# Kernel optimization log

Hardware: AMD Instinct MI355X
Metric: run time of the kernel (lower is better)

The kernel has to match this reference:

```python
import jax, jax.numpy as jnp
import numpy as np

N_HEAD = 16
D_MODEL = 1024
D_HEAD = D_MODEL // N_HEAD
B, T = 2, 2048


def setup_inputs() -> dict:
    key = jax.random.key(0)
    k1, k2, k3 = jax.random.split(key, 3)
    x = jax.random.normal(k1, (B, T, D_MODEL), dtype=jnp.float32)
    w_attn = jax.random.normal(k2, (3 * D_MODEL, D_MODEL), dtype=jnp.float32) * (D_MODEL ** -0.5)
    w_proj = jax.random.normal(k3, (D_MODEL, D_MODEL), dtype=jnp.float32) * (D_MODEL ** -0.5)
    return {"x": x, "w_attn": w_attn, "w_proj": w_proj}


def _rms_norm(x):
    eps = jnp.asarray(jnp.finfo(x.dtype).eps, x.dtype)
    var = jnp.mean(jnp.square(x), axis=-1, keepdims=True)
    return x * jax.lax.rsqrt(var + eps)


def _rotate_half(x):
    x1, x2 = jnp.split(x, 2, axis=-1)
    return jnp.concatenate((-x2, x1), axis=-1)


def reference(x, w_attn, w_proj):
    Bx, Tx, C = x.shape
    qkv = jnp.einsum('btc,fc->btf', x, w_attn)  # [B,T,3C]
    q, k, v = jnp.split(qkv, 3, axis=-1)
    # [B, H, T, Dh]
    q = q.reshape(Bx, Tx, N_HEAD, D_HEAD).transpose(0, 2, 1, 3)
    k = k.reshape(Bx, Tx, N_HEAD, D_HEAD).transpose(0, 2, 1, 3)
    v = v.reshape(Bx, Tx, N_HEAD, D_HEAD).transpose(0, 2, 1, 3)
    # QK RMSNorm (no learned weight)
    q = _rms_norm(q)
    k = _rms_norm(k)
    # Rotary embedding over full d_head: freqs tiled twice
    inv_freq = 1.0 / (10000.0 ** (jnp.arange(0, D_HEAD, 2, dtype=jnp.float32) / D_HEAD))
    t = jnp.arange(Tx, dtype=jnp.float32)
    freqs = jnp.einsum('i,j->ij', t, inv_freq)  # [T, Dh/2]
    emb = jnp.concatenate((freqs, freqs), axis=-1)  # [T, Dh]
    cos = jnp.cos(emb)[None, None, :, :]
    sin = jnp.sin(emb)[None, None, :, :]
    q = q * cos + _rotate_half(q) * sin
    k = k * cos + _rotate_half(k) * sin
    # Causal SDPA
    scale = D_HEAD ** -0.5
    scores = jnp.einsum('bhqd,bhkd->bhqk', q, k) * scale
    causal = jnp.tril(jnp.ones((Tx, Tx), dtype=bool))
    scores = jnp.where(causal[None, None], scores, jnp.asarray(-jnp.inf, scores.dtype))
    attn = jax.nn.softmax(scores, axis=-1)
    y = jnp.einsum('bhqk,bhkd->bhqd', attn, v)
    y = y.transpose(0, 2, 1, 3).reshape(Bx, Tx, C)
    return jnp.einsum('btc,oc->bto', y, w_proj)
```

## Files before the change

kernel.cpp:

```cpp
#include <hip/hip_runtime.h>
#include <cstdint>
#include <cstddef>


typedef short bf16x8 __attribute__((ext_vector_type(8)));
typedef float floatx4 __attribute__((ext_vector_type(4)));
typedef unsigned short ushortx8 __attribute__((ext_vector_type(8)));
typedef unsigned short ushortx4 __attribute__((ext_vector_type(4)));

#define DEVI __device__ __forceinline__

DEVI float bf2f(unsigned short u) {
    unsigned int x = ((unsigned int)u) << 16;
    return __builtin_bit_cast(float, x);
}
DEVI unsigned short f2bf(float f) {
    unsigned int u = __builtin_bit_cast(unsigned int, f);
    u += 0x7fffu + ((u >> 16) & 1u);
    return (unsigned short)(u >> 16);
}

DEVI void glds16(const unsigned short* g, unsigned short* l) {
    __builtin_amdgcn_global_load_lds(
        (const __attribute__((address_space(1))) unsigned int*)g,
        (__attribute__((address_space(3))) unsigned int*)l, 16, 0, 0);
}

DEVI void cast8(unsigned short* dst, const float* src) {
    floatx4 a = *(const floatx4*)src;
    floatx4 b = *(const floatx4*)(src + 4);
    ushortx8 o;
    o[0] = f2bf(a[0]); o[1] = f2bf(a[1]); o[2] = f2bf(a[2]); o[3] = f2bf(a[3]);
    o[4] = f2bf(b[0]); o[5] = f2bf(b[1]); o[6] = f2bf(b[2]); o[7] = f2bf(b[3]);
    *(ushortx8*)dst = o;
}

__global__ __launch_bounds__(256)
void cast_inputs(const float* __restrict__ x, const float* __restrict__ wa,
                 const float* __restrict__ wp,
                 unsigned short* __restrict__ xb, unsigned short* __restrict__ wab,
                 unsigned short* __restrict__ wpb)
{
    size_t g = (size_t)blockIdx.x * 256 + threadIdx.x;
    size_t stride = (size_t)gridDim.x * 256;
    for (size_t i = g; i < (4194304 / 8); i += stride) cast8(xb  + i * 8, x  + i * 8);
    for (size_t i = g; i < (3145728 / 8); i += stride) cast8(wab + i * 8, wa + i * 8);
    for (size_t i = g; i < (1048576 / 8); i += stride) cast8(wpb + i * 8, wp + i * 8);
}

template <bool QKV_SPLIT, int BN>
__global__ __launch_bounds__(256)
void gemm_bt(const unsigned short* __restrict__ A, const unsigned short* __restrict__ B,
             unsigned short* __restrict__ Cqk, float* __restrict__ Cf,
             unsigned short* __restrict__ Vt, int M, int N, int K)
{
    constexpr int WCOLS = (BN == 128) ? 2 : 1;
    constexpr int WROWS = 4 / WCOLS;
    constexpr int MI    = 128 / (16 * WROWS);

    __shared__ __align__(16) unsigned short As[128 * 32];
    __shared__ __align__(16) unsigned short Bs[BN * 32];

    const int tid  = threadIdx.x;
    const int lane = tid & 63;
    const int w    = tid >> 6;
    const int wm   = w / WCOLS, wn = w % WCOLS;
    const int quad = lane >> 4;
    const int lm   = lane & 15;
    const int m0 = blockIdx.y * 128;
    const int n0 = blockIdx.x * BN;
    const int sr = lane >> 2;
    const int sc = (lane & 3) * 8;

    floatx4 acc[MI][4] = {};

    for (int k0 = 0; k0 < K; k0 += 32) {
        __syncthreads();
        #pragma unroll
        for (int i = 0; i < 2; ++i) {
            int r = w * 32 + i * 16;
            glds16(&A[(size_t)(m0 + r + sr) * K + k0 + sc], &As[r * 32]);
        }
        #pragma unroll
        for (int i = 0; i < BN / 64; ++i) {
            int r = w * (BN / 4) + i * 16;
            glds16(&B[(size_t)(n0 + r + sr) * K + k0 + sc], &Bs[r * 32]);
        }
        __syncthreads();

        bf16x8 a[MI];
        #pragma unroll
        for (int i = 0; i < MI; ++i)
            a[i] = *(const bf16x8*)&As[(wm * (16 * MI) + i * 16 + lm) * 32 + quad * 8];
        #pragma unroll
        for (int j = 0; j < 4; ++j) {
            bf16x8 b = *(const bf16x8*)&Bs[(wn * 64 + j * 16 + lm) * 32 + quad * 8];
            #pragma unroll
            for (int i = 0; i < MI; ++i)
                acc[i][j] = __builtin_amdgcn_mfma_f32_16x16x32_bf16(a[i], b, acc[i][j], 0, 0, 0);
        }
    }

    #pragma unroll
    for (int i = 0; i < MI; ++i) {
        #pragma unroll
        for (int j = 0; j < 4; ++j) {
            int col = n0 + wn * 64 + j * 16 + lm;
            #pragma unroll
            for (int r = 0; r < 4; ++r) {
                int row = m0 + wm * (16 * MI) + i * 16 + quad * 4 + r;
                if constexpr (QKV_SPLIT) {
                    unsigned short v = f2bf(acc[i][j][r]);
                    if (col < 2048) {
                        Cqk[(size_t)row * 2048 + col] = v;
                    } else {
                        int bq = row >> 11, t = row & 2047;
                        Vt[((size_t)(bq * 1024 + (col - 2048))) * 2048 + t] = v;
                    }
                } else {
                    Cf[(size_t)row * N + col] = acc[i][j][r];
                }
            }
        }
    }
}

__global__ __launch_bounds__(256)
void rmsnorm_rope(unsigned short* __restrict__ qk)
{
    int gw   = (blockIdx.x * 256 + threadIdx.x) >> 6;
    int lane = threadIdx.x & 63;
    int h = gw & 15;
    int t = (gw >> 4) & 2047;
    int b = gw >> 15;

    size_t base = ((size_t)(b * 2048 + t)) * 2048 + h * 64 + lane;
    float q = bf2f(qk[base]);
    float k = bf2f(qk[base + 1024]);

    float sq = q * q, sk = k * k;
    #pragma unroll
    for (int off = 32; off >= 1; off >>= 1) {
        sq += __shfl_xor(sq, off, 64);
        sk += __shfl_xor(sk, off, 64);
    }
    const float eps = 1.1920929e-07f;
    q *= rsqrtf(sq * (1.0f / 64.0f) + eps);
    k *= rsqrtf(sk * (1.0f / 64.0f) + eps);

    int i = lane & 31;
    float ang = (float)t * expf(-(float)i * 0.28782313662425572f);
    float c = cosf(ang), s = sinf(ang);
    float qp = __shfl_xor(q, 32, 64);
    float kp = __shfl_xor(k, 32, 64);
    float sgn = (lane < 32) ? -1.0f : 1.0f;
    float qo = q * c + sgn * qp * s;
    float ko = k * c + sgn * kp * s;

    qk[base]        = f2bf(qo);
    qk[base + 1024] = f2bf(ko);
}

__global__ __launch_bounds__(256)
void attention(const unsigned short* __restrict__ qk,
               const unsigned short* __restrict__ Vt,
               unsigned short* __restrict__ Y)
{
    constexpr int LD = 72;
    __shared__ __align__(16) unsigned short QPs[64 * LD];
    __shared__ __align__(16) unsigned short Ks [64 * LD];
    __shared__ __align__(16) unsigned short Vs [64 * LD];

    const int tid  = threadIdx.x;
    const int lane = tid & 63;
    const int w    = tid >> 6;
    const int quad = lane >> 4;
    const int lm   = lane & 15;

    const int bh = blockIdx.x;
    const int b  = bh >> 4, h = bh & 15;

    const unsigned short* kbase = qk + (size_t)b * 2048 * 2048 + 1024 + h * 64;
    const unsigned short* vbase = Vt + (size_t)bh * 64 * 2048;

    #pragma unroll
    for (int sel = 0; sel < 2; ++sel) {
        const int qt = sel ? (int)blockIdx.y : 31 - (int)blockIdx.y;
        const int q0 = qt * 64;
        const int qrow = q0 + w * 16 + lm;

        if (sel) __syncthreads();

        #pragma unroll
        for (int i = 0; i < 2; ++i) {
            int c = i * 256 + tid, row = c >> 3, col = (c & 7) * 8;
            *(ushortx8*)&QPs[row * LD + col] =
                *(const ushortx8*)&qk[((size_t)(b * 2048 + q0 + row)) * 2048 + h * 64 + col];
        }

        ushortx8 kreg[2], vreg[2];
        #pragma unroll
        for (int i = 0; i < 2; ++i) {
            int c = i * 256 + tid, row = c >> 3, col = (c & 7) * 8;
            kreg[i] = *(const ushortx8*)&kbase[(size_t)row * 2048 + col];
            vreg[i] = *(const ushortx8*)&vbase[(size_t)row * 2048 + col];
        }

        floatx4 o[4] = {};
        float lsum = 0.0f;
        bf16x8 qf[2];
        const float c1 = 0.125f * 1.44269504f;
        const float c2 = 8.0f   * 1.44269504f;

        for (int kt = 0; kt <= qt; ++kt) {
            const int k0 = kt * 64;
            __syncthreads();
            #pragma unroll
            for (int i = 0; i < 2; ++i) {
                int c = i * 256 + tid, row = c >> 3, col = (c & 7) * 8;
                *(ushortx8*)&Ks[row * LD + col] = kreg[i];
                *(ushortx8*)&Vs[row * LD + col] = vreg[i];
            }
            __syncthreads();

            if (kt == 0) {
                #pragma unroll
                for (int kk = 0; kk < 2; ++kk)
                    qf[kk] = *(const bf16x8*)&QPs[(w * 16 + lm) * LD + kk * 32 + quad * 8];
            }
            if (kt < qt) {
                const int kn = k0 + 64;
                #pragma unroll
                for (int i = 0; i < 2; ++i) {
                    int c = i * 256 + tid, row = c >> 3, col = (c & 7) * 8;
                    kreg[i] = *(const ushortx8*)&kbase[(size_t)(kn + row) * 2048 + col];
                    vreg[i] = *(const ushortx8*)&vbase[(size_t)row * 2048 + kn + col];
                }
            }

            floatx4 sa[4] = {};
            #pragma unroll
            for (int kk = 0; kk < 2; ++kk) {
                #pragma unroll
                for (int j = 0; j < 4; ++j) {
                    bf16x8 kf = *(const bf16x8*)&Ks[(j * 16 + lm) * LD + kk * 32 + quad * 8];
                    sa[j] = __builtin_amdgcn_mfma_f32_16x16x32_bf16(kf, qf[kk], sa[j], 0, 0, 0);
                }
            }

            const bool dg = (kt == qt);
            #pragma unroll
            for (int j = 0; j < 4; ++j) {
                int kb = k0 + j * 16 + quad * 4;
                ushortx4 pk;
                #pragma unroll
                for (int r = 0; r < 4; ++r) {
                    float p = exp2f(sa[j][r] * c1 - c2);
                    if (dg && (kb + r) > qrow) p = 0.0f;
                    lsum += p;
                    pk[r] = f2bf(p);
                }
                *(ushortx4*)&QPs[(w * 16 + lm) * LD + j * 16 + quad * 4] = pk;
            }

            #pragma unroll
            for (int kk = 0; kk < 2; ++kk) {
                bf16x8 pf = *(const bf16x8*)&QPs[(w * 16 + lm) * LD + kk * 32 + quad * 8];
                #pragma unroll
                for (int j = 0; j < 4; ++j) {
                    bf16x8 vf = *(const bf16x8*)&Vs[(j * 16 + lm) * LD + kk * 32 + quad * 8];
                    o[j] = __builtin_amdgcn_mfma_f32_16x16x32_bf16(pf, vf, o[j], 0, 0, 0);
                }
            }
        }

        float lt = lsum;
        lt += __shfl_xor(lt, 16, 64);
        lt += __shfl_xor(lt, 32, 64);
        float rv = 1.0f / lt;
        float rinv[4];
        #pragma unroll
        for (int r = 0; r < 4; ++r)
            rinv[r] = __shfl(rv, (quad << 4) + quad * 4 + r, 64);

        #pragma unroll
        for (int j = 0; j < 4; ++j) {
            int colg = h * 64 + j * 16 + lm;
            #pragma unroll
            for (int r = 0; r < 4; ++r) {
                int rowg = q0 + w * 16 + quad * 4 + r;
                Y[((size_t)(b * 2048 + rowg)) * 1024 + colg] = f2bf(o[j][r] * rinv[r]);
            }
        }
    }
}

extern "C" void kernel_launch(void* const* d_in, const int* in_sizes, int n_in,
                              void* d_out, int out_size, void* d_ws, size_t ws_size,
                              hipStream_t stream)
{
    const float* x      = (const float*)d_in[0];
    const float* w_attn = (const float*)d_in[1];
    const float* w_proj = (const float*)d_in[2];
    float* out = (float*)d_out;

    unsigned short* qkbuf = (unsigned short*)d_ws;
    unsigned short* Vtb   = qkbuf + (size_t)4096 * 2048;
    unsigned short* y     = Vtb   + (size_t)32 * 64 * 2048;
    unsigned short* wpb   = y     + (size_t)4096 * 1024;
    unsigned short* xb  = (unsigned short*)d_out;
    unsigned short* wab = xb + (size_t)4096 * 1024;

    dim3 blk(256);
    cast_inputs<<<dim3(1024), blk, 0, stream>>>(x, w_attn, w_proj, xb, wab, wpb);
    gemm_bt<true, 128>
        <<<dim3(24, 32), blk, 0, stream>>>(xb, wab, qkbuf, nullptr, Vtb, 4096, 3072, 1024);
    rmsnorm_rope<<<dim3(16384), blk, 0, stream>>>(qkbuf);
    attention<<<dim3(32, 16), blk, 0, stream>>>(qkbuf, Vtb, y);
    gemm_bt<false, 64>
        <<<dim3(16, 32), blk, 0, stream>>>(y, wpb, nullptr, out, nullptr, 4096, 1024, 1024);
}
```

Baseline: 209.5 us.

## Restructure attention to one query tile per block with MFMA row sums

The attention kernel no longer pairs two query tiles per block. It launches one block per query tile, doubling the grid, and peels the diagonal tile out of the loop so the causal masking check only runs there. Row sums of P are computed with an extra MFMA against a ones vector, bf16 packing uses a cheaper round-half-up perm path, and the V-transpose store in the QKV GEMM epilogue becomes a vectorized 4-element write. Dropping the pairing removes the load balancing it provided, so per-block work becomes uneven, and the bf16 rounding of P changes slightly.

```diff
diff --git a/kernel.cpp b/kernel.cpp
--- a/kernel.cpp
+++ b/kernel.cpp
@@ -7,6 +7,7 @@
 typedef float floatx4 __attribute__((ext_vector_type(4)));
 typedef unsigned short ushortx8 __attribute__((ext_vector_type(8)));
 typedef unsigned short ushortx4 __attribute__((ext_vector_type(4)));
+typedef unsigned int uintx2 __attribute__((ext_vector_type(2)));
 
 #define DEVI __device__ __forceinline__
 
@@ -18,6 +19,11 @@
     unsigned int u = __builtin_bit_cast(unsigned int, f);
     u += 0x7fffu + ((u >> 16) & 1u);
     return (unsigned short)(u >> 16);
+}
+DEVI unsigned int pkbf2(float a, float b) {
+    unsigned int ua = __builtin_bit_cast(unsigned int, a) + 0x8000u;
+    unsigned int ub = __builtin_bit_cast(unsigned int, b) + 0x8000u;
+    return __builtin_amdgcn_perm(ub, ua, 0x07060302);
 }
 
 DEVI void glds16(const unsigned short* g, unsigned short* l) {
@@ -106,20 +112,23 @@
         #pragma unroll
         for (int j = 0; j < 4; ++j) {
             int col = n0 + wn * 64 + j * 16 + lm;
-            #pragma unroll
-            for (int r = 0; r < 4; ++r) {
-                int row = m0 + wm * (16 * MI) + i * 16 + quad * 4 + r;
-                if constexpr (QKV_SPLIT) {
-                    unsigned short v = f2bf(acc[i][j][r]);
-                    if (col < 2048) {
-                        Cqk[(size_t)row * 2048 + col] = v;
-                    } else {
-                        int bq = row >> 11, t = row & 2047;
-                        Vt[((size_t)(bq * 1024 + (col - 2048))) * 2048 + t] = v;
-                    }
+            int row0 = m0 + wm * (16 * MI) + i * 16 + quad * 4;
+            if constexpr (QKV_SPLIT) {
+                if (col < 2048) {
+                    #pragma unroll
+                    for (int r = 0; r < 4; ++r)
+                        Cqk[(size_t)(row0 + r) * 2048 + col] = f2bf(acc[i][j][r]);
                 } else {
-                    Cf[(size_t)row * N + col] = acc[i][j][r];
+                    int bq = row0 >> 11, t0 = row0 & 2047;
+                    ushortx4 pk;
+                    #pragma unroll
+                    for (int r = 0; r < 4; ++r) pk[r] = f2bf(acc[i][j][r]);
+                    *(ushortx4*)&Vt[((size_t)(bq * 1024 + (col - 2048))) * 2048 + t0] = pk;
                 }
+            } else {
+                #pragma unroll
+                for (int r = 0; r < 4; ++r)
+                    Cf[(size_t)(row0 + r) * N + col] = acc[i][j][r];
             }
         }
     }
@@ -178,119 +187,144 @@
     const int lm   = lane & 15;
 
     const int bh = blockIdx.x;
+    const int qt = 31 - blockIdx.y;
     const int b  = bh >> 4, h = bh & 15;
-
-    const unsigned short* kbase = qk + (size_t)b * 2048 * 2048 + 1024 + h * 64;
-    const unsigned short* vbase = Vt + (size_t)bh * 64 * 2048;
-
-    #pragma unroll
-    for (int sel = 0; sel < 2; ++sel) {
-        const int qt = sel ? (int)blockIdx.y : 31 - (int)blockIdx.y;
-        const int q0 = qt * 64;
-        const int qrow = q0 + w * 16 + lm;
-
-        if (sel) __syncthreads();
-
-        #pragma unroll
-        for (int i = 0; i < 2; ++i) {
-            int c = i * 256 + tid, row = c >> 3, col = (c & 7) * 8;
-            *(ushortx8*)&QPs[row * LD + col] =
-                *(const ushortx8*)&qk[((size_t)(b * 2048 + q0 + row)) * 2048 + h * 64 + col];
-        }
-
-        ushortx8 kreg[2], vreg[2];
-        #pragma unroll
-        for (int i = 0; i < 2; ++i) {
-            int c = i * 256 + tid, row = c >> 3, col = (c & 7) * 8;
-            kreg[i] = *(const ushortx8*)&kbase[(size_t)row * 2048 + col];
-            vreg[i] = *(const ushortx8*)&vbase[(size_t)row * 2048 + col];
-        }
-
-        floatx4 o[4] = {};
-        float lsum = 0.0f;
-        bf16x8 qf[2];
-        const float c1 = 0.125f * 1.44269504f;
-        const float c2 = 8.0f   * 1.44269504f;
-
-        for (int kt = 0; kt <= qt; ++kt) {
-            const int k0 = kt * 64;
-            __syncthreads();
-            #pragma unroll
-            for (int i = 0; i < 2; ++i) {
-                int c = i * 256 + tid, row = c >> 3, col = (c & 7) * 8;
-                *(ushortx8*)&Ks[row * LD + col] = kreg[i];
-                *(ushortx8*)&Vs[row * LD + col] = vreg[i];
-            }
-            __syncthreads();
-
-            if (kt == 0) {
-                #pragma unroll
-                for (int kk = 0; kk < 2; ++kk)
-                    qf[kk] = *(const bf16x8*)&QPs[(w * 16 + lm) * LD + kk * 32 + quad * 8];
-            }
-            if (kt < qt) {
-                const int kn = k0 + 64;
-                #pragma unroll
-                for (int i = 0; i < 2; ++i) {
-                    int c = i * 256 + tid, row = c >> 3, col = (c & 7) * 8;
-                    kreg[i] = *(const ushortx8*)&kbase[(size_t)(kn + row) * 2048 + col];
-                    vreg[i] = *(const ushortx8*)&vbase[(size_t)row * 2048 + kn + col];
-                }
-            }
-
-            floatx4 sa[4] = {};
-            #pragma unroll
-            for (int kk = 0; kk < 2; ++kk) {
-                #pragma unroll
-                for (int j = 0; j < 4; ++j) {
-                    bf16x8 kf = *(const bf16x8*)&Ks[(j * 16 + lm) * LD + kk * 32 + quad * 8];
-                    sa[j] = __builtin_amdgcn_mfma_f32_16x16x32_bf16(kf, qf[kk], sa[j], 0, 0, 0);
-                }
-            }
-
-            const bool dg = (kt == qt);
+    const int q0 = qt * 64;
+    const int qrow = q0 + w * 16 + lm;
+
+    const int r0 = tid >> 3, r1 = r0 + 32, pc = (tid & 7) * 8;
+    const unsigned short* kp0 = qk + (size_t)b * 2048 * 2048 + 1024 + h * 64
+                              + (size_t)r0 * 2048 + pc;
+    const unsigned short* kp1 = kp0 + (size_t)32 * 2048;
+    const unsigned short* vp0 = Vt + (size_t)bh * 64 * 2048 + (size_t)r0 * 2048 + pc;
+    const unsigned short* vp1 = vp0 + (size_t)32 * 2048;
+
+    #pragma unroll
+    for (int i = 0; i < 2; ++i) {
+        int c = i * 256 + tid, row = c >> 3, col = (c & 7) * 8;
+        *(ushortx8*)&QPs[row * LD + col] =
+            *(const ushortx8*)&qk[((size_t)(b * 2048 + q0 + row)) * 2048 + h * 64 + col];
+    }
+
+    ushortx8 kreg0 = *(const ushortx8*)kp0, kreg1 = *(const ushortx8*)kp1;
+    ushortx8 vreg0 = *(const ushortx8*)vp0, vreg1 = *(const ushortx8*)vp1;
+    kp0 += (size_t)64 * 2048; kp1 += (size_t)64 * 2048;
+    vp0 += 64; vp1 += 64;
+
+    __syncthreads();
+    bf16x8 qf[2];
+    #pragma unroll
+    for (int kk = 0; kk < 2; ++kk)
+        qf[kk] = *(const bf16x8*)&QPs[(w * 16 + lm) * LD + kk * 32 + quad * 8];
+
+    bf16x8 ones;
+    #pragma unroll
+    for (int i = 0; i < 8; ++i) ones[i] = (short)0x3F80;
+
+    floatx4 o[4] = {};
+    floatx4 l_acc = {};
+    const float c1 = 0.125f * 1.44269504f;
+    const float c2 = 8.0f   * 1.44269504f;
+
+    for (int kt = 0; kt < qt; ++kt) {
+        __syncthreads();
+        *(ushortx8*)&Ks[r0 * LD + pc] = kreg0;
+        *(ushortx8*)&Ks[r1 * LD + pc] = kreg1;
+        *(ushortx8*)&Vs[r0 * LD + pc] = vreg0;
+        *(ushortx8*)&Vs[r1 * LD + pc] = vreg1;
+        __syncthreads();
+
+        kreg0 = *(const ushortx8*)kp0; kreg1 = *(const ushortx8*)kp1;
+        vreg0 = *(const ushortx8*)vp0; vreg1 = *(const ushortx8*)vp1;
+        kp0 += (size_t)64 * 2048; kp1 += (size_t)64 * 2048;
+        vp0 += 64; vp1 += 64;
+
+        floatx4 sa[4] = {};
+        #pragma unroll
+        for (int kk = 0; kk < 2; ++kk)
             #pragma unroll
             for (int j = 0; j < 4; ++j) {
-                int kb = k0 + j * 16 + quad * 4;
-                ushortx4 pk;
-                #pragma unroll
-                for (int r = 0; r < 4; ++r) {
-                    float p = exp2f(sa[j][r] * c1 - c2);
-                    if (dg && (kb + r) > qrow) p = 0.0f;
-                    lsum += p;
-                    pk[r] = f2bf(p);
-                }
-                *(ushortx4*)&QPs[(w * 16 + lm) * LD + j * 16 + quad * 4] = pk;
-            }
-
-            #pragma unroll
-            for (int kk = 0; kk < 2; ++kk) {
-                bf16x8 pf = *(const bf16x8*)&QPs[(w * 16 + lm) * LD + kk * 32 + quad * 8];
-                #pragma unroll
-                for (int j = 0; j < 4; ++j) {
-                    bf16x8 vf = *(const bf16x8*)&Vs[(j * 16 + lm) * LD + kk * 32 + quad * 8];
-                    o[j] = __builtin_amdgcn_mfma_f32_16x16x32_bf16(pf, vf, o[j], 0, 0, 0);
-                }
-            }
-        }
-
-        float lt = lsum;
-        lt += __shfl_xor(lt, 16, 64);
-        lt += __shfl_xor(lt, 32, 64);
-        float rv = 1.0f / lt;
-        float rinv[4];
-        #pragma unroll
-        for (int r = 0; r < 4; ++r)
-            rinv[r] = __shfl(rv, (quad << 4) + quad * 4 + r, 64);
+                bf16x8 kf = *(const bf16x8*)&Ks[(j * 16 + lm) * LD + kk * 32 + quad * 8];
+                sa[j] = __builtin_amdgcn_mfma_f32_16x16x32_bf16(kf, qf[kk], sa[j], 0, 0, 0);
+            }
 
         #pragma unroll
         for (int j = 0; j < 4; ++j) {
-            int colg = h * 64 + j * 16 + lm;
-            #pragma unroll
-            for (int r = 0; r < 4; ++r) {
-                int rowg = q0 + w * 16 + quad * 4 + r;
-                Y[((size_t)(b * 2048 + rowg)) * 1024 + colg] = f2bf(o[j][r] * rinv[r]);
-            }
+            float p0 = exp2f(sa[j][0] * c1 - c2);
+            float p1 = exp2f(sa[j][1] * c1 - c2);
+            float p2 = exp2f(sa[j][2] * c1 - c2);
+            float p3 = exp2f(sa[j][3] * c1 - c2);
+            uintx2 pk;
+            pk[0] = pkbf2(p0, p1);
+            pk[1] = pkbf2(p2, p3);
+            *(uintx2*)&QPs[(w * 16 + lm) * LD + j * 16 + quad * 4] = pk;
+        }
+
+        #pragma unroll
+        for (int kk = 0; kk < 2; ++kk) {
+            bf16x8 pf = *(const bf16x8*)&QPs[(w * 16 + lm) * LD + kk * 32 + quad * 8];
+            #pragma unroll
+            for (int j = 0; j < 4; ++j) {
+                bf16x8 vf = *(const bf16x8*)&Vs[(j * 16 + lm) * LD + kk * 32 + quad * 8];
+                o[j] = __builtin_amdgcn_mfma_f32_16x16x32_bf16(pf, vf, o[j], 0, 0, 0);
+            }
+            l_acc = __builtin_amdgcn_mfma_f32_16x16x32_bf16(pf, ones, l_acc, 0, 0, 0);
+        }
+    }
+
+    {
+        __syncthreads();
+        *(ushortx8*)&Ks[r0 * LD + pc] = kreg0;
+        *(ushortx8*)&Ks[r1 * LD + pc] = kreg1;
+        *(ushortx8*)&Vs[r0 * LD + pc] = vreg0;
+        *(ushortx8*)&Vs[r1 * LD + pc] = vreg1;
+        __syncthreads();
+
+        floatx4 sa[4] = {};
+        #pragma unroll
+        for (int kk = 0; kk < 2; ++kk)
+            #pragma unroll
+            for (int j = 0; j < 4; ++j) {
+                bf16x8 kf = *(const bf16x8*)&Ks[(j * 16 + lm) * LD + kk * 32 + quad * 8];
+                sa[j] = __builtin_amdgcn_mfma_f32_16x16x32_bf16(kf, qf[kk], sa[j], 0, 0, 0);
+            }
+
+        #pragma unroll
+        for (int j = 0; j < 4; ++j) {
+            int kb = q0 + j * 16 + quad * 4;
+            float p0 = (kb + 0 > qrow) ? 0.0f : exp2f(sa[j][0] * c1 - c2);
+            float p1 = (kb + 1 > qrow) ? 0.0f : exp2f(sa[j][1] * c1 - c2);
+            float p2 = (kb + 2 > qrow) ? 0.0f : exp2f(sa[j][2] * c1 - c2);
+            float p3 = (kb + 3 > qrow) ? 0.0f : exp2f(sa[j][3] * c1 - c2);
+            uintx2 pk;
+            pk[0] = pkbf2(p0, p1);
+            pk[1] = pkbf2(p2, p3);
+            *(uintx2*)&QPs[(w * 16 + lm) * LD + j * 16 + quad * 4] = pk;
+        }
+
+        #pragma unroll
+        for (int kk = 0; kk < 2; ++kk) {
+            bf16x8 pf = *(const bf16x8*)&QPs[(w * 16 + lm) * LD + kk * 32 + quad * 8];
+            #pragma unroll
+            for (int j = 0; j < 4; ++j) {
+                bf16x8 vf = *(const bf16x8*)&Vs[(j * 16 + lm) * LD + kk * 32 + quad * 8];
+                o[j] = __builtin_amdgcn_mfma_f32_16x16x32_bf16(pf, vf, o[j], 0, 0, 0);
+            }
+            l_acc = __builtin_amdgcn_mfma_f32_16x16x32_bf16(pf, ones, l_acc, 0, 0, 0);
+        }
+    }
+
+    float rinv[4];
+    #pragma unroll
+    for (int r = 0; r < 4; ++r) rinv[r] = 1.0f / l_acc[r];
+
+    #pragma unroll
+    for (int j = 0; j < 4; ++j) {
+        int colg = h * 64 + j * 16 + lm;
+        #pragma unroll
+        for (int r = 0; r < 4; ++r) {
+            int rowg = q0 + w * 16 + quad * 4 + r;
+            Y[((size_t)(b * 2048 + rowg)) * 1024 + colg] = f2bf(o[j][r] * rinv[r]);
         }
     }
 }
@@ -316,7 +350,7 @@
     gemm_bt<true, 128>
         <<<dim3(24, 32), blk, 0, stream>>>(xb, wab, qkbuf, nullptr, Vtb, 4096, 3072, 1024);
     rmsnorm_rope<<<dim3(16384), blk, 0, stream>>>(qkbuf);
-    attention<<<dim3(32, 16), blk, 0, stream>>>(qkbuf, Vtb, y);
+    attention<<<dim3(32, 32), blk, 0, stream>>>(qkbuf, Vtb, y);
     gemm_bt<false, 64>
         <<<dim3(16, 32), blk, 0, stream>>>(y, wpb, nullptr, out, nullptr, 4096, 1024, 1024);
 }
```

Result: faster. 196.0 us (-6.5%).
